# Kernel tuning notes

Measured on AMD Instinct MI355X. Metric: run time of the kernel, lower is better.

Reference implementation:

```python
import jax, jax.numpy as jnp
import numpy as np

B, N, D, H = 4096, 64, 32, 64

def setup_inputs() -> dict:
    key = jax.random.key(0)
    ks = jax.random.split(key, 10)
    s = lambda fan_in: 1.0 / np.sqrt(fan_in)
    return {
        "joint_features": jax.random.normal(ks[0], (B, N, D), jnp.float32),
        "Wm1": jax.random.uniform(ks[1], (2 * D, H), jnp.float32, -s(2 * D), s(2 * D)),
        "bm1": jax.random.uniform(ks[2], (H,), jnp.float32, -s(2 * D), s(2 * D)),
        "Wm2": jax.random.uniform(ks[3], (H, D), jnp.float32, -s(H), s(H)),
        "bm2": jax.random.uniform(ks[4], (D,), jnp.float32, -s(H), s(H)),
        "Wu1": jax.random.uniform(ks[5], (2 * D, H), jnp.float32, -s(2 * D), s(2 * D)),
        "bu1": jax.random.uniform(ks[6], (H,), jnp.float32, -s(2 * D), s(2 * D)),
        "Wu2": jax.random.uniform(ks[7], (H, D), jnp.float32, -s(H), s(H)),
        "bu2": jax.random.uniform(ks[8], (D,), jnp.float32, -s(H), s(H)),
        "residual_weight": jnp.float32(0.5),
        "num_joints": N,
    }

def reference(joint_features, Wm1, bm1, Wm2, bm2, Wu1, bu1, Wu2, bu2, residual_weight, num_joints):
    n = num_joints
    # chain topology: directed edges (i->i+1) and (i+1->i); dst receives message
    dst = jnp.concatenate([jnp.arange(n - 1), jnp.arange(1, n)])  # [E]
    src = jnp.concatenate([jnp.arange(1, n), jnp.arange(n - 1)])  # [E]
    # edge gather + concat: [B, E, 2D]
    edge_in = jnp.concatenate([joint_features[:, dst], joint_features[:, src]], axis=-1)
    # message MLP (ReLU after both layers, per original Sequential)
    msg = jax.nn.relu(jax.nn.relu(edge_in @ Wm1 + bm1) @ Wm2 + bm2)  # [B, E, D]
    # scatter-add messages to destination nodes
    messages = jnp.zeros_like(joint_features).at[:, dst].add(msg)  # [B, N, D]
    # per-node update MLP on concat(feature, message)
    upd_in = jnp.concatenate([joint_features, messages], axis=-1)  # [B, N, 2D]
    updated = jax.nn.relu(upd_in @ Wu1 + bu1) @ Wu2 + bu2  # [B, N, D]
    return residual_weight * updated + (1.0 - residual_weight) * joint_features
```

## Files before the change

kernel.cpp:

```cpp
#include <hip/hip_runtime.h>
#include <hip/hip_bf16.h>


typedef __bf16 bf16x8 __attribute__((ext_vector_type(8)));
typedef float  f32x4  __attribute__((ext_vector_type(4)));

#define NB 2
#define ROWS  (NB * 64)
#define EROWS (NB * 128)
#define PQ_S 136
#define MB_S 40
#define HU_S 72

typedef unsigned short u16;

__device__ __forceinline__ u16 f2b(float f) {
    return __builtin_bit_cast(u16, (__bf16)f);
}
__device__ __forceinline__ f32x4 MFMA(bf16x8 a, bf16x8 b, f32x4 c) {
    return __builtin_amdgcn_mfma_f32_16x16x32_bf16(a, b, c, 0, 0, 0);
}

__global__ __launch_bounds__(256, 2)
void agn_mfma(const float* __restrict__ x, const float* __restrict__ Wm1,
              const float* __restrict__ bm1, const float* __restrict__ Wm2,
              const float* __restrict__ bm2, const float* __restrict__ Wu1,
              const float* __restrict__ bu1, const float* __restrict__ Wu2,
              const float* __restrict__ bu2, const float* __restrict__ rw_p,
              float* __restrict__ out)
{
    __shared__ __align__(16) u16 sPQ[ROWS * PQ_S];
    __shared__ __align__(16) u16 sMB[EROWS * MB_S];
    u16* sHU = sPQ;

    const int t = threadIdx.x;
    const int w = t >> 6;
    const int lane = t & 63;
    const int ln = lane & 15;
    const int q  = lane >> 4;

    const size_t blk = (size_t)blockIdx.x * (NB * 64 * 32);
    const float* xb = x + blk;
    float*       ob = out + blk;

    bf16x8 B1[8];
#pragma unroll
    for (int nt = 0; nt < 8; ++nt) {
        const int koff = (nt < 4) ? 0 : 32;
        const int wcol = (nt & 3) * 16 + ln;
#pragma unroll
        for (int j = 0; j < 8; ++j)
            B1[nt][j] = (__bf16)Wm1[(koff + q * 8 + j) * 64 + wcol];
    }
#pragma unroll
    for (int m = 0; m < 2; ++m) {
        const int mt = 2 * w + m;
        const int row = mt * 16 + ln;
        const float* xr = xb + row * 32 + q * 8;
        float4 a0 = *(const float4*)xr;
        float4 a1 = *(const float4*)(xr + 4);
        bf16x8 A = {(__bf16)a0.x, (__bf16)a0.y, (__bf16)a0.z, (__bf16)a0.w,
                    (__bf16)a1.x, (__bf16)a1.y, (__bf16)a1.z, (__bf16)a1.w};
#pragma unroll
        for (int nt = 0; nt < 8; ++nt) {
            f32x4 acc = {0.f, 0.f, 0.f, 0.f};
            acc = MFMA(A, B1[nt], acc);
            const int crow = mt * 16 + q * 4;
            const int ccol = nt * 16 + ln;
#pragma unroll
            for (int r = 0; r < 4; ++r)
                sPQ[(crow + r) * PQ_S + ccol] = f2b(acc[r]);
        }
    }

    float bm1v[2][8];
    bf16x8 B2[2][2];
#pragma unroll
    for (int s = 0; s < 2; ++s) {
#pragma unroll
        for (int j = 0; j < 8; ++j)
            bm1v[s][j] = bm1[s * 32 + q * 8 + j];
#pragma unroll
        for (int nt = 0; nt < 2; ++nt)
#pragma unroll
            for (int j = 0; j < 8; ++j)
                B2[s][nt][j] = (__bf16)Wm2[(s * 32 + q * 8 + j) * 32 + nt * 16 + ln];
    }
    float bm2v[2] = { bm2[ln], bm2[16 + ln] };
    __syncthreads();

#pragma unroll
    for (int m = 0; m < 4; ++m) {
        const int mt = 4 * w + m;
        const int erow = mt * 16 + ln;
        const int bb = erow >> 7;
        int e = erow & 127;
        if (e >= 126) e = 0;
        const int dst  = (e < 63) ? e : e - 62;
        const int srcn = (e < 63) ? e + 1 : e - 63;
        const int pd = (bb << 6) + dst;
        const int ps = (bb << 6) + srcn;
        bf16x8 A2[2];
#pragma unroll
        for (int s = 0; s < 2; ++s) {
            const int k0 = s * 32 + q * 8;
            uint4 u1 = *(const uint4*)&sPQ[pd * PQ_S + k0];
            uint4 u2 = *(const uint4*)&sPQ[ps * PQ_S + 64 + k0];
            const unsigned* p1 = (const unsigned*)&u1;
            const unsigned* p2 = (const unsigned*)&u2;
#pragma unroll
            for (int h = 0; h < 4; ++h) {
                float lo = __uint_as_float(p1[h] << 16) +
                           __uint_as_float(p2[h] << 16) + bm1v[s][2 * h];
                float hi = __uint_as_float(p1[h] & 0xFFFF0000u) +
                           __uint_as_float(p2[h] & 0xFFFF0000u) + bm1v[s][2 * h + 1];
                A2[s][2 * h]     = (__bf16)fmaxf(lo, 0.f);
                A2[s][2 * h + 1] = (__bf16)fmaxf(hi, 0.f);
            }
        }
#pragma unroll
        for (int nt = 0; nt < 2; ++nt) {
            f32x4 acc = {0.f, 0.f, 0.f, 0.f};
            acc = MFMA(A2[0], B2[0][nt], acc);
            acc = MFMA(A2[1], B2[1][nt], acc);
            const int crow = mt * 16 + q * 4;
            const int ccol = nt * 16 + ln;
#pragma unroll
            for (int r = 0; r < 4; ++r)
                sMB[(crow + r) * MB_S + ccol] = f2b(fmaxf(acc[r] + bm2v[nt], 0.f));
        }
    }

    bf16x8 B3[2][4];
#pragma unroll
    for (int s = 0; s < 2; ++s)
#pragma unroll
        for (int nt = 0; nt < 4; ++nt)
#pragma unroll
            for (int j = 0; j < 8; ++j)
                B3[s][nt][j] = (__bf16)Wu1[(s * 32 + q * 8 + j) * 64 + nt * 16 + ln];
    float bu1v[4] = { bu1[ln], bu1[16 + ln], bu1[32 + ln], bu1[48 + ln] };
    __syncthreads();

#pragma unroll
    for (int m = 0; m < 2; ++m) {
        const int mt = 2 * w + m;
        const int row = mt * 16 + ln;
        const int bb = row >> 6;
        const int i2 = row & 63;
        const float* xr = xb + row * 32 + q * 8;
        float4 a0 = *(const float4*)xr;
        float4 a1 = *(const float4*)(xr + 4);
        bf16x8 A0 = {(__bf16)a0.x, (__bf16)a0.y, (__bf16)a0.z, (__bf16)a0.w,
                     (__bf16)a1.x, (__bf16)a1.y, (__bf16)a1.z, (__bf16)a1.w};
        float mv[8] = {0.f, 0.f, 0.f, 0.f, 0.f, 0.f, 0.f, 0.f};
        if (i2 < 63) {
            uint4 u = *(const uint4*)&sMB[(bb * 128 + i2) * MB_S + q * 8];
            const unsigned* p = (const unsigned*)&u;
#pragma unroll
            for (int h = 0; h < 4; ++h) {
                mv[2 * h]     += __uint_as_float(p[h] << 16);
                mv[2 * h + 1] += __uint_as_float(p[h] & 0xFFFF0000u);
            }
        }
        if (i2 > 0) {
            uint4 u = *(const uint4*)&sMB[(bb * 128 + 62 + i2) * MB_S + q * 8];
            const unsigned* p = (const unsigned*)&u;
#pragma unroll
            for (int h = 0; h < 4; ++h) {
                mv[2 * h]     += __uint_as_float(p[h] << 16);
                mv[2 * h + 1] += __uint_as_float(p[h] & 0xFFFF0000u);
            }
        }
        bf16x8 A1;
#pragma unroll
        for (int j = 0; j < 8; ++j) A1[j] = (__bf16)mv[j];
#pragma unroll
        for (int nt = 0; nt < 4; ++nt) {
            f32x4 acc = {0.f, 0.f, 0.f, 0.f};
            acc = MFMA(A0, B3[0][nt], acc);
            acc = MFMA(A1, B3[1][nt], acc);
            const int crow = mt * 16 + q * 4;
            const int ccol = nt * 16 + ln;
#pragma unroll
            for (int r = 0; r < 4; ++r)
                sHU[(crow + r) * HU_S + ccol] = f2b(fmaxf(acc[r] + bu1v[nt], 0.f));
        }
    }

    bf16x8 B4[2][2];
#pragma unroll
    for (int s = 0; s < 2; ++s)
#pragma unroll
        for (int nt = 0; nt < 2; ++nt)
#pragma unroll
            for (int j = 0; j < 8; ++j)
                B4[s][nt][j] = (__bf16)Wu2[(s * 32 + q * 8 + j) * 32 + nt * 16 + ln];
    float bu2v[2] = { bu2[ln], bu2[16 + ln] };
    const float rw = rw_p[0];
    const float omrw = 1.f - rw;
    __syncthreads();

#pragma unroll
    for (int m = 0; m < 2; ++m) {
        const int mt = 2 * w + m;
        const int arow = mt * 16 + ln;
        bf16x8 A[2];
#pragma unroll
        for (int s = 0; s < 2; ++s) {
            uint4 u = *(const uint4*)&sHU[arow * HU_S + s * 32 + q * 8];
            A[s] = __builtin_bit_cast(bf16x8, u);
        }
#pragma unroll
        for (int nt = 0; nt < 2; ++nt) {
            f32x4 acc = {0.f, 0.f, 0.f, 0.f};
            acc = MFMA(A[0], B4[0][nt], acc);
            acc = MFMA(A[1], B4[1][nt], acc);
            const int crow = mt * 16 + q * 4;
            const int ccol = nt * 16 + ln;
#pragma unroll
            for (int r = 0; r < 4; ++r) {
                const int off = (crow + r) * 32 + ccol;
                ob[off] = rw * (acc[r] + bu2v[nt]) + omrw * xb[off];
            }
        }
    }
}

extern "C" void kernel_launch(void* const* d_in, const int* in_sizes, int n_in,
                              void* d_out, int out_size, void* d_ws, size_t ws_size,
                              hipStream_t stream) {
    const float* x   = (const float*)d_in[0];
    const float* Wm1 = (const float*)d_in[1];
    const float* bm1 = (const float*)d_in[2];
    const float* Wm2 = (const float*)d_in[3];
    const float* bm2 = (const float*)d_in[4];
    const float* Wu1 = (const float*)d_in[5];
    const float* bu1 = (const float*)d_in[6];
    const float* Wu2 = (const float*)d_in[7];
    const float* bu2 = (const float*)d_in[8];
    const float* rw  = (const float*)d_in[9];
    float* out = (float*)d_out;

    const int B = in_sizes[0] / (64 * 32);
    agn_mfma<<<B / NB, 256, 0, stream>>>(x, Wm1, bm1, Wm2, bm2, Wu1, bu1, Wu2, bu2, rw, out);
}
```

Measured before the change: 125.2 us.

## Loop multiple batch chunks per block and compute edge layer directly from gathered inputs

```diff
diff --git a/kernel.cpp b/kernel.cpp
--- a/kernel.cpp
+++ b/kernel.cpp
@@ -4,21 +4,22 @@
 
 typedef __bf16 bf16x8 __attribute__((ext_vector_type(8)));
 typedef float  f32x4  __attribute__((ext_vector_type(4)));
-
-#define NB 2
-#define ROWS  (NB * 64)
-#define EROWS (NB * 128)
-#define PQ_S 136
-#define MB_S 40
-#define HU_S 72
-
 typedef unsigned short u16;
 
-__device__ __forceinline__ u16 f2b(float f) {
-    return __builtin_bit_cast(u16, (__bf16)f);
-}
+#define NBATCH 8
+#define NBI 2
+#define ITERS (NBATCH / NBI)
+#define HS  72
+#define MBS 40
+
+__device__ __forceinline__ u16 f2b(float f) { return __builtin_bit_cast(u16, (__bf16)f); }
 __device__ __forceinline__ f32x4 MFMA(bf16x8 a, bf16x8 b, f32x4 c) {
     return __builtin_amdgcn_mfma_f32_16x16x32_bf16(a, b, c, 0, 0, 0);
+}
+__device__ __forceinline__ bf16x8 pack8(float4 a, float4 b) {
+    bf16x8 r = {(__bf16)a.x, (__bf16)a.y, (__bf16)a.z, (__bf16)a.w,
+                (__bf16)b.x, (__bf16)b.y, (__bf16)b.z, (__bf16)b.w};
+    return r;
 }
 
 __global__ __launch_bounds__(256, 2)
@@ -29,9 +30,8 @@
               const float* __restrict__ bu2, const float* __restrict__ rw_p,
               float* __restrict__ out)
 {
-    __shared__ __align__(16) u16 sPQ[ROWS * PQ_S];
-    __shared__ __align__(16) u16 sMB[EROWS * MB_S];
-    u16* sHU = sPQ;
+    __shared__ __align__(16) u16 sH[256 * HS];
+    __shared__ __align__(16) u16 sMB[256 * MBS];
 
     const int t = threadIdx.x;
     const int w = t >> 6;
@@ -39,99 +39,21 @@
     const int ln = lane & 15;
     const int q  = lane >> 4;
 
-    const size_t blk = (size_t)blockIdx.x * (NB * 64 * 32);
-    const float* xb = x + blk;
-    float*       ob = out + blk;
-
-    bf16x8 B1[8];
-#pragma unroll
-    for (int nt = 0; nt < 8; ++nt) {
-        const int koff = (nt < 4) ? 0 : 32;
-        const int wcol = (nt & 3) * 16 + ln;
-#pragma unroll
-        for (int j = 0; j < 8; ++j)
-            B1[nt][j] = (__bf16)Wm1[(koff + q * 8 + j) * 64 + wcol];
-    }
-#pragma unroll
-    for (int m = 0; m < 2; ++m) {
-        const int mt = 2 * w + m;
-        const int row = mt * 16 + ln;
-        const float* xr = xb + row * 32 + q * 8;
-        float4 a0 = *(const float4*)xr;
-        float4 a1 = *(const float4*)(xr + 4);
-        bf16x8 A = {(__bf16)a0.x, (__bf16)a0.y, (__bf16)a0.z, (__bf16)a0.w,
-                    (__bf16)a1.x, (__bf16)a1.y, (__bf16)a1.z, (__bf16)a1.w};
-#pragma unroll
-        for (int nt = 0; nt < 8; ++nt) {
-            f32x4 acc = {0.f, 0.f, 0.f, 0.f};
-            acc = MFMA(A, B1[nt], acc);
-            const int crow = mt * 16 + q * 4;
-            const int ccol = nt * 16 + ln;
-#pragma unroll
-            for (int r = 0; r < 4; ++r)
-                sPQ[(crow + r) * PQ_S + ccol] = f2b(acc[r]);
-        }
-    }
-
-    float bm1v[2][8];
-    bf16x8 B2[2][2];
-#pragma unroll
-    for (int s = 0; s < 2; ++s) {
-#pragma unroll
-        for (int j = 0; j < 8; ++j)
-            bm1v[s][j] = bm1[s * 32 + q * 8 + j];
+    bf16x8 B1a[4], B1b[4], B2[2][2], B3[2][4], B4[2][2];
+#pragma unroll
+    for (int nt = 0; nt < 4; ++nt)
+#pragma unroll
+        for (int j = 0; j < 8; ++j) {
+            B1a[nt][j] = (__bf16)Wm1[(q * 8 + j) * 64 + nt * 16 + ln];
+            B1b[nt][j] = (__bf16)Wm1[(32 + q * 8 + j) * 64 + nt * 16 + ln];
+        }
+#pragma unroll
+    for (int s = 0; s < 2; ++s)
 #pragma unroll
         for (int nt = 0; nt < 2; ++nt)
 #pragma unroll
             for (int j = 0; j < 8; ++j)
                 B2[s][nt][j] = (__bf16)Wm2[(s * 32 + q * 8 + j) * 32 + nt * 16 + ln];
-    }
-    float bm2v[2] = { bm2[ln], bm2[16 + ln] };
-    __syncthreads();
-
-#pragma unroll
-    for (int m = 0; m < 4; ++m) {
-        const int mt = 4 * w + m;
-        const int erow = mt * 16 + ln;
-        const int bb = erow >> 7;
-        int e = erow & 127;
-        if (e >= 126) e = 0;
-        const int dst  = (e < 63) ? e : e - 62;
-        const int srcn = (e < 63) ? e + 1 : e - 63;
-        const int pd = (bb << 6) + dst;
-        const int ps = (bb << 6) + srcn;
-        bf16x8 A2[2];
-#pragma unroll
-        for (int s = 0; s < 2; ++s) {
-            const int k0 = s * 32 + q * 8;
-            uint4 u1 = *(const uint4*)&sPQ[pd * PQ_S + k0];
-            uint4 u2 = *(const uint4*)&sPQ[ps * PQ_S + 64 + k0];
-            const unsigned* p1 = (const unsigned*)&u1;
-            const unsigned* p2 = (const unsigned*)&u2;
-#pragma unroll
-            for (int h = 0; h < 4; ++h) {
-                float lo = __uint_as_float(p1[h] << 16) +
-                           __uint_as_float(p2[h] << 16) + bm1v[s][2 * h];
-                float hi = __uint_as_float(p1[h] & 0xFFFF0000u) +
-                           __uint_as_float(p2[h] & 0xFFFF0000u) + bm1v[s][2 * h + 1];
-                A2[s][2 * h]     = (__bf16)fmaxf(lo, 0.f);
-                A2[s][2 * h + 1] = (__bf16)fmaxf(hi, 0.f);
-            }
-        }
-#pragma unroll
-        for (int nt = 0; nt < 2; ++nt) {
-            f32x4 acc = {0.f, 0.f, 0.f, 0.f};
-            acc = MFMA(A2[0], B2[0][nt], acc);
-            acc = MFMA(A2[1], B2[1][nt], acc);
-            const int crow = mt * 16 + q * 4;
-            const int ccol = nt * 16 + ln;
-#pragma unroll
-            for (int r = 0; r < 4; ++r)
-                sMB[(crow + r) * MB_S + ccol] = f2b(fmaxf(acc[r] + bm2v[nt], 0.f));
-        }
-    }
-
-    bf16x8 B3[2][4];
 #pragma unroll
     for (int s = 0; s < 2; ++s)
 #pragma unroll
@@ -139,56 +61,6 @@
 #pragma unroll
             for (int j = 0; j < 8; ++j)
                 B3[s][nt][j] = (__bf16)Wu1[(s * 32 + q * 8 + j) * 64 + nt * 16 + ln];
-    float bu1v[4] = { bu1[ln], bu1[16 + ln], bu1[32 + ln], bu1[48 + ln] };
-    __syncthreads();
-
-#pragma unroll
-    for (int m = 0; m < 2; ++m) {
-        const int mt = 2 * w + m;
-        const int row = mt * 16 + ln;
-        const int bb = row >> 6;
-        const int i2 = row & 63;
-        const float* xr = xb + row * 32 + q * 8;
-        float4 a0 = *(const float4*)xr;
-        float4 a1 = *(const float4*)(xr + 4);
-        bf16x8 A0 = {(__bf16)a0.x, (__bf16)a0.y, (__bf16)a0.z, (__bf16)a0.w,
-                     (__bf16)a1.x, (__bf16)a1.y, (__bf16)a1.z, (__bf16)a1.w};
-        float mv[8] = {0.f, 0.f, 0.f, 0.f, 0.f, 0.f, 0.f, 0.f};
-        if (i2 < 63) {
-            uint4 u = *(const uint4*)&sMB[(bb * 128 + i2) * MB_S + q * 8];
-            const unsigned* p = (const unsigned*)&u;
-#pragma unroll
-            for (int h = 0; h < 4; ++h) {
-                mv[2 * h]     += __uint_as_float(p[h] << 16);
-                mv[2 * h + 1] += __uint_as_float(p[h] & 0xFFFF0000u);
-            }
-        }
-        if (i2 > 0) {
-            uint4 u = *(const uint4*)&sMB[(bb * 128 + 62 + i2) * MB_S + q * 8];
-            const unsigned* p = (const unsigned*)&u;
-#pragma unroll
-            for (int h = 0; h < 4; ++h) {
-                mv[2 * h]     += __uint_as_float(p[h] << 16);
-                mv[2 * h + 1] += __uint_as_float(p[h] & 0xFFFF0000u);
-            }
-        }
-        bf16x8 A1;
-#pragma unroll
-        for (int j = 0; j < 8; ++j) A1[j] = (__bf16)mv[j];
-#pragma unroll
-        for (int nt = 0; nt < 4; ++nt) {
-            f32x4 acc = {0.f, 0.f, 0.f, 0.f};
-            acc = MFMA(A0, B3[0][nt], acc);
-            acc = MFMA(A1, B3[1][nt], acc);
-            const int crow = mt * 16 + q * 4;
-            const int ccol = nt * 16 + ln;
-#pragma unroll
-            for (int r = 0; r < 4; ++r)
-                sHU[(crow + r) * HU_S + ccol] = f2b(fmaxf(acc[r] + bu1v[nt], 0.f));
-        }
-    }
-
-    bf16x8 B4[2][2];
 #pragma unroll
     for (int s = 0; s < 2; ++s)
 #pragma unroll
@@ -196,34 +68,144 @@
 #pragma unroll
             for (int j = 0; j < 8; ++j)
                 B4[s][nt][j] = (__bf16)Wu2[(s * 32 + q * 8 + j) * 32 + nt * 16 + ln];
-    float bu2v[2] = { bu2[ln], bu2[16 + ln] };
+
+    float bm1v[4], bu1v[4], bm2v[2], bu2v[2];
+#pragma unroll
+    for (int nt = 0; nt < 4; ++nt) { bm1v[nt] = bm1[nt * 16 + ln]; bu1v[nt] = bu1[nt * 16 + ln]; }
+#pragma unroll
+    for (int nt = 0; nt < 2; ++nt) { bm2v[nt] = bm2[nt * 16 + ln]; bu2v[nt] = bu2[nt * 16 + ln]; }
     const float rw = rw_p[0];
-    const float omrw = 1.f - rw;
-    __syncthreads();
-
-#pragma unroll
-    for (int m = 0; m < 2; ++m) {
-        const int mt = 2 * w + m;
-        const int arow = mt * 16 + ln;
-        bf16x8 A[2];
-#pragma unroll
-        for (int s = 0; s < 2; ++s) {
-            uint4 u = *(const uint4*)&sHU[arow * HU_S + s * 32 + q * 8];
-            A[s] = __builtin_bit_cast(bf16x8, u);
-        }
-#pragma unroll
-        for (int nt = 0; nt < 2; ++nt) {
-            f32x4 acc = {0.f, 0.f, 0.f, 0.f};
-            acc = MFMA(A[0], B4[0][nt], acc);
-            acc = MFMA(A[1], B4[1][nt], acc);
-            const int crow = mt * 16 + q * 4;
-            const int ccol = nt * 16 + ln;
-#pragma unroll
-            for (int r = 0; r < 4; ++r) {
-                const int off = (crow + r) * 32 + ccol;
-                ob[off] = rw * (acc[r] + bu2v[nt]) + omrw * xb[off];
-            }
-        }
+    const float om = 1.f - rw;
+
+    const size_t base = (size_t)blockIdx.x * (NBATCH * 64 * 32);
+
+    for (int it = 0; it < ITERS; ++it) {
+        const float* xit = x + base + (size_t)it * (NBI * 64 * 32);
+        float*       oit = out + base + (size_t)it * (NBI * 64 * 32);
+
+        {
+            float4 xd[4][2], xsv[4][2];
+#pragma unroll
+            for (int m = 0; m < 4; ++m) {
+                const int mt = 4 * w + m;
+                const int erow = mt * 16 + ln;
+                const int bb = erow >> 7;
+                int e = erow & 127;
+                if (e >= 126) e = 0;
+                const int dst  = (e < 63) ? e : e - 62;
+                const int srcn = (e < 63) ? e + 1 : e - 63;
+                const float* pd = xit + ((bb << 6) + dst) * 32 + q * 8;
+                const float* ps = xit + ((bb << 6) + srcn) * 32 + q * 8;
+                xd[m][0] = *(const float4*)pd;  xd[m][1] = *(const float4*)(pd + 4);
+                xsv[m][0] = *(const float4*)ps; xsv[m][1] = *(const float4*)(ps + 4);
+            }
+#pragma unroll
+            for (int m = 0; m < 4; ++m) {
+                const int mt = 4 * w + m;
+                bf16x8 Ad = pack8(xd[m][0], xd[m][1]);
+                bf16x8 As = pack8(xsv[m][0], xsv[m][1]);
+#pragma unroll
+                for (int nt = 0; nt < 4; ++nt) {
+                    f32x4 acc = {0.f, 0.f, 0.f, 0.f};
+                    acc = MFMA(Ad, B1a[nt], acc);
+                    acc = MFMA(As, B1b[nt], acc);
+                    const int rb = mt * 16 + q * 4;
+                    const int c  = nt * 16 + ln;
+#pragma unroll
+                    for (int r = 0; r < 4; ++r)
+                        sH[(rb + r) * HS + c] = f2b(fmaxf(acc[r] + bm1v[nt], 0.f));
+                }
+            }
+        }
+        __syncthreads();
+
+#pragma unroll
+        for (int m = 0; m < 4; ++m) {
+            const int mt = 4 * w + m;
+            const int row = mt * 16 + ln;
+            bf16x8 A0 = __builtin_bit_cast(bf16x8, *(const uint4*)&sH[row * HS + q * 8]);
+            bf16x8 A1 = __builtin_bit_cast(bf16x8, *(const uint4*)&sH[row * HS + 32 + q * 8]);
+#pragma unroll
+            for (int nt = 0; nt < 2; ++nt) {
+                f32x4 acc = {0.f, 0.f, 0.f, 0.f};
+                acc = MFMA(A0, B2[0][nt], acc);
+                acc = MFMA(A1, B2[1][nt], acc);
+                const int rb = mt * 16 + q * 4;
+                const int c  = nt * 16 + ln;
+#pragma unroll
+                for (int r = 0; r < 4; ++r)
+                    sMB[(rb + r) * MBS + c] = f2b(fmaxf(acc[r] + bm2v[nt], 0.f));
+            }
+        }
+        __syncthreads();
+
+#pragma unroll
+        for (int m = 0; m < 2; ++m) {
+            const int mt = 2 * w + m;
+            const int row = mt * 16 + ln;
+            const int bb = row >> 6;
+            const int i2 = row & 63;
+            const float* p = xit + row * 32 + q * 8;
+            float4 a0 = *(const float4*)p;
+            float4 a1 = *(const float4*)(p + 4);
+            bf16x8 A0 = pack8(a0, a1);
+            float mv[8] = {0.f, 0.f, 0.f, 0.f, 0.f, 0.f, 0.f, 0.f};
+            if (i2 < 63) {
+                uint4 u = *(const uint4*)&sMB[((bb << 7) + i2) * MBS + q * 8];
+                const unsigned* pu = (const unsigned*)&u;
+#pragma unroll
+                for (int h = 0; h < 4; ++h) {
+                    mv[2 * h]     += __uint_as_float(pu[h] << 16);
+                    mv[2 * h + 1] += __uint_as_float(pu[h] & 0xFFFF0000u);
+                }
+            }
+            if (i2 > 0) {
+                uint4 u = *(const uint4*)&sMB[((bb << 7) + 62 + i2) * MBS + q * 8];
+                const unsigned* pu = (const unsigned*)&u;
+#pragma unroll
+                for (int h = 0; h < 4; ++h) {
+                    mv[2 * h]     += __uint_as_float(pu[h] << 16);
+                    mv[2 * h + 1] += __uint_as_float(pu[h] & 0xFFFF0000u);
+                }
+            }
+            bf16x8 A1;
+#pragma unroll
+            for (int j = 0; j < 8; ++j) A1[j] = (__bf16)mv[j];
+#pragma unroll
+            for (int nt = 0; nt < 4; ++nt) {
+                f32x4 acc = {0.f, 0.f, 0.f, 0.f};
+                acc = MFMA(A0, B3[0][nt], acc);
+                acc = MFMA(A1, B3[1][nt], acc);
+                const int rb = mt * 16 + q * 4;
+                const int c  = nt * 16 + ln;
+#pragma unroll
+                for (int r = 0; r < 4; ++r)
+                    sH[(rb + r) * HS + c] = f2b(fmaxf(acc[r] + bu1v[nt], 0.f));
+            }
+        }
+        __syncthreads();
+
+#pragma unroll
+        for (int m = 0; m < 2; ++m) {
+            const int mt = 2 * w + m;
+            const int arow = mt * 16 + ln;
+            bf16x8 A0 = __builtin_bit_cast(bf16x8, *(const uint4*)&sH[arow * HS + q * 8]);
+            bf16x8 A1 = __builtin_bit_cast(bf16x8, *(const uint4*)&sH[arow * HS + 32 + q * 8]);
+#pragma unroll
+            for (int nt = 0; nt < 2; ++nt) {
+                f32x4 acc = {0.f, 0.f, 0.f, 0.f};
+                acc = MFMA(A0, B4[0][nt], acc);
+                acc = MFMA(A1, B4[1][nt], acc);
+                const int rb = mt * 16 + q * 4;
+                const int c  = nt * 16 + ln;
+#pragma unroll
+                for (int r = 0; r < 4; ++r) {
+                    const int off = (rb + r) * 32 + c;
+                    oit[off] = rw * (acc[r] + bu2v[nt]) + om * xit[off];
+                }
+            }
+        }
+        __syncthreads();
     }
 }
 
@@ -243,5 +225,5 @@
     float* out = (float*)d_out;
 
     const int B = in_sizes[0] / (64 * 32);
-    agn_mfma<<<B / NB, 256, 0, stream>>>(x, Wm1, bm1, Wm2, bm2, Wu1, bu1, Wu2, bu2, rw, out);
-}
+    agn_mfma<<<B / NBATCH, 256, 0, stream>>>(x, Wm1, bm1, Wm2, bm2, Wu1, bu1, Wu2, bu2, rw, out);
+}
```

Result: faster. 121.7 us (-2.8%).
